# Kernel optimization log

Hardware: AMD Instinct MI355X
Metric: run time of the kernel (lower is better)

## Reference

```python
import jax, jax.numpy as jnp
import numpy as np

BN_EPS = 1e-5


def setup_inputs() -> dict:
    key = jax.random.key(0)
    ks = jax.random.split(key, 5)
    B, T, N, C, O, K, E = 2, 4, 50000, 32, 32, 3, 800000
    x = jax.random.normal(ks[0], (B, T, N, C), dtype=jnp.float32)
    edge_index = jax.random.randint(ks[1], (2, E), 0, N, dtype=jnp.int64)
    edge_weight = jax.random.uniform(ks[2], (E,), dtype=jnp.float32)
    W = jax.random.normal(ks[3], (K, C, O), dtype=jnp.float32) * 0.05
    bias = jnp.zeros((O,), dtype=jnp.float32)
    gamma = jnp.ones((O,), dtype=jnp.float32)
    beta = jnp.zeros((O,), dtype=jnp.float32)
    return {"x": x, "edge_index": edge_index, "edge_weight": edge_weight,
            "W": W, "bias": bias, "gamma": gamma, "beta": beta}


def reference(x, edge_index, edge_weight, W, bias, gamma, beta):
    # x: [B, T, N, C]; edge_index: [2, E]; W: [K, C, O]
    B, T, N, C = x.shape
    K = W.shape[0]
    src, dst = edge_index[0], edge_index[1]

    # Scaled Laplacian L_hat = 2L/lambda_max - I with sym norm, lambda_max=2
    # => L_hat = -D^{-1/2} A D^{-1/2} (zero diagonal), PyG ChebConv default.
    deg = jax.ops.segment_sum(edge_weight, src, num_segments=N)
    safe = jnp.where(deg > 0, deg, 1.0)
    dinv = jnp.where(deg > 0, 1.0 / jnp.sqrt(safe), 0.0)
    norm = -dinv[src] * edge_weight * dinv[dst]  # [E]

    # Batch all (b, t) slices together: [N, M, C] with M = B*T
    xn = jnp.transpose(x, (2, 0, 1, 3)).reshape(N, B * T, C)

    def lap(z):  # sparse SpMM applied to every (b,t) slice at once
        return jax.ops.segment_sum(norm[:, None, None] * z[src], dst,
                                   num_segments=N)

    # Chebyshev recursion: T0 = x, T1 = L_hat x, Tk = 2 L_hat T_{k-1} - T_{k-2}
    Tx_prev2 = xn
    out = jnp.einsum('nmc,co->nmo', Tx_prev2, W[0])
    if K > 1:
        Tx_prev = lap(xn)
        out = out + jnp.einsum('nmc,co->nmo', Tx_prev, W[1])
        for k in range(2, K):
            Tx_k = 2.0 * lap(Tx_prev) - Tx_prev2
            out = out + jnp.einsum('nmc,co->nmo', Tx_k, W[k])
            Tx_prev2, Tx_prev = Tx_prev, Tx_k
    out = out + bias  # [N, M, O]

    # BatchNorm1d in training mode, applied per (b,t) slice over nodes,
    # exactly as the original per-slice loop does (biased variance).
    mean = jnp.mean(out, axis=0, keepdims=True)              # [1, M, O]
    var = jnp.mean((out - mean) ** 2, axis=0, keepdims=True)  # [1, M, O]
    y = gamma * (out - mean) * jax.lax.rsqrt(var + BN_EPS) + beta
    y = jax.nn.relu(y)

    return jnp.transpose(y.reshape(N, B, T, -1), (1, 2, 0, 3))  # [B,T,N,O]
```

## Files before the change

### kernel.cpp

```cpp
#include <hip/hip_runtime.h>

#define NNODES 50000
#define NEDGES 800000
#define MB 8
#define CF 32
#define OF 32
#define FPN 256
#define TOTAL_OUT (MB * NNODES * OF)
#define NREP 8

#define BSH 9
#define BINW 512
#define NB ((NNODES + BINW - 1) / BINW)
#define BINCAP 9216
#define NBB 128
#define EPB (NEDGES / NBB)
#define CAPL 32
#define CH 16

typedef unsigned short ushort_t;
typedef unsigned int uint_t;
typedef __attribute__((ext_vector_type(8))) short bf16x8;
typedef __attribute__((ext_vector_type(4))) float f32x4;

__device__ __forceinline__ ushort_t f2bf(float f) {
    uint_t u = __float_as_uint(f);
    u += 0x7FFFu + ((u >> 16) & 1u);
    return (ushort_t)(u >> 16);
}
__device__ __forceinline__ float bflo(uint_t u) { return __uint_as_float(u << 16); }
__device__ __forceinline__ float bfhi(uint_t u) { return __uint_as_float(u & 0xFFFF0000u); }

__device__ __forceinline__ bool detect_is64(const int* ei) {
    int lane = threadIdx.x & 63;
    int v = ei[2 * lane + 1];
    return __ballot(v != 0) == 0ULL;
}

__global__ void __launch_bounds__(256) k_build(const int* __restrict__ ei,
                                               const float* __restrict__ w,
                                               const float* __restrict__ x,
                                               float* __restrict__ deg8,
                                               int* __restrict__ g_bin_cnt,
                                               int2* __restrict__ binbuf,
                                               ushort_t* __restrict__ xn) {
    int blk = blockIdx.x;
    int t = threadIdx.x;
    __shared__ int l_cnt[NB];
    __shared__ int2 l_buf[NB][CAPL];
    if (blk < NBB) {
        bool is64 = detect_is64(ei);
        for (int i = t; i < NB; i += 256) l_cnt[i] = 0;
        __syncthreads();
        int e0 = blk * EPB;
        int eend = e0 + EPB;
        for (int base = e0; base < eend; base += 256) {
            int e = base + t;
            if (e < eend) {
                int s = is64 ? ei[2 * e] : ei[e];
                int d = is64 ? ei[2 * (NEDGES + e)] : ei[NEDGES + e];
                float wt = w[e];
                atomicAdd(&deg8[s * NREP + ((e >> 8) & 7)], wt);
                int bin = d >> BSH;
                int2 entry;
                entry.x = s | ((d & (BINW - 1)) << 16);
                entry.y = __float_as_int(wt);
                int pos = atomicAdd(&l_cnt[bin], 1);
                if (pos < CAPL) {
                    l_buf[bin][pos] = entry;
                } else {
                    int gp = atomicAdd(&g_bin_cnt[bin], 1);
                    if (gp < BINCAP) binbuf[(size_t)bin * BINCAP + gp] = entry;
                }
            }
            __syncthreads();
            bool last = (base + 256 >= eend);
            if (t < NB) {
                int c = min(l_cnt[t], CAPL);
                int nflush = last ? c : (c & ~(CH - 1));
                if (nflush > 0) {
                    int gp = atomicAdd(&g_bin_cnt[t], nflush);
                    int2* dst = binbuf + (size_t)t * BINCAP;
                    for (int i = 0; i < nflush; i++) {
                        int p = gp + i;
                        if (p < BINCAP) dst[p] = l_buf[t][i];
                    }
                }
                int r = c - nflush;
                for (int i = 0; i < r; i++) l_buf[t][i] = l_buf[t][nflush + i];
                l_cnt[t] = r;
            }
            __syncthreads();
        }
    } else {
        int bb = blk - NBB;
        int lane = t & 63;
        int n = bb * 4 + (t >> 6);
        int m = lane >> 3;
        int c = (4 * lane) & 31;
        const float4 v = *(const float4*)(x + ((size_t)m * NNODES + n) * CF + c);
        uint2 d;
        d.x = (uint_t)f2bf(v.x) | ((uint_t)f2bf(v.y) << 16);
        d.y = (uint_t)f2bf(v.z) | ((uint_t)f2bf(v.w) << 16);
        *(uint2*)(xn + (size_t)n * FPN + 4 * lane) = d;
    }
}

__global__ void __launch_bounds__(256) k_csr(const int* __restrict__ g_bin_cnt,
                                             const int2* __restrict__ binbuf,
                                             int2* __restrict__ csr,
                                             int* __restrict__ csr_off) {
    __shared__ int l_ncnt[BINW];
    __shared__ int l_off[BINW];
    __shared__ int l_ws[4];
    __shared__ int l_red[4];
    int b = blockIdx.x;
    int t = threadIdx.x;
    int lane = t & 63, wv = t >> 6;

    int vb = (t < b) ? min(g_bin_cnt[t], BINCAP) : 0;
    #pragma unroll
    for (int off = 32; off >= 1; off >>= 1) vb += __shfl_down(vb, off);
    if (lane == 0) l_red[wv] = vb;
    l_ncnt[t] = 0;
    l_ncnt[t + 256] = 0;
    __syncthreads();
    int base = l_red[0] + l_red[1] + l_red[2] + l_red[3];

    int cnt = min(g_bin_cnt[b], BINCAP);
    const int2* bp = binbuf + (size_t)b * BINCAP;
    for (int i = t; i < cnt; i += 256) {
        int dl = bp[i].x >> 16;
        atomicAdd(&l_ncnt[dl], 1);
    }
    __syncthreads();

    int a0 = l_ncnt[2 * t], a1 = l_ncnt[2 * t + 1];
    int psum = a0 + a1;
    int v = psum;
    #pragma unroll
    for (int off = 1; off < 64; off <<= 1) {
        int u = __shfl_up(v, off);
        if (lane >= off) v += u;
    }
    if (lane == 63) l_ws[wv] = v;
    __syncthreads();
    int wpre = 0;
    for (int i = 0; i < wv; i++) wpre += l_ws[i];
    int excl = wpre + v - psum;
    l_off[2 * t] = excl;
    l_off[2 * t + 1] = excl + a0;
    __syncthreads();

    int n0 = b * BINW;
    for (int i = t; i < BINW; i += 256) {
        int n = n0 + i;
        if (n < NNODES) csr_off[n] = base + l_off[i];
    }
    if (b == NB - 1 && t == 0) csr_off[NNODES] = base + cnt;
    __syncthreads();

    for (int i = t; i < cnt; i += 256) {
        int2 e = bp[i];
        int dl = e.x >> 16;
        int slot = atomicAdd(&l_off[dl], 1);
        int2 o;
        o.x = e.x & 0xFFFF;
        o.y = e.y;
        csr[(size_t)base + slot] = o;
    }
}

__global__ void k_dinv(const float* __restrict__ deg8, float* __restrict__ dinv) {
    int n = blockIdx.x * blockDim.x + threadIdx.x;
    if (n >= NNODES) return;
    const float4* p = (const float4*)(deg8 + (size_t)n * NREP);
    float4 a = p[0], b = p[1];
    float s = a.x + a.y + a.z + a.w + b.x + b.y + b.z + b.w;
    dinv[n] = (s > 0.0f) ? (1.0f / sqrtf(s)) : 0.0f;
}

template <int PHASE>
__global__ void __launch_bounds__(256) k_spmm(const ushort_t* __restrict__ src,
                                              const ushort_t* __restrict__ xn0,
                                              const int* __restrict__ csr_off,
                                              const int2* __restrict__ csr,
                                              const float* __restrict__ dinv,
                                              ushort_t* __restrict__ dst) {
    int t = threadIdx.x;
    int lane = t & 63;
    int n = __builtin_amdgcn_readfirstlane(blockIdx.x * 4 + (t >> 6));
    int off = csr_off[n];
    int cnt = min(csr_off[n + 1] - off, 64);
    float dn = dinv[n];
    float a0 = 0.0f, a1 = 0.0f, a2 = 0.0f, a3 = 0.0f;
    if (cnt > 0) {
        int j = off + min(lane, cnt - 1);
        int2 ed = csr[j];
        int cv = ed.x;
        float vw = -dinv[cv] * __int_as_float(ed.y) * dn;
        uint_t vv = __float_as_uint(vw);
        for (int k = 0; k < cnt; k += 16) {
            int sc[16]; float v[16];
            #pragma unroll
            for (int i = 0; i < 16; i++) {
                sc[i] = __builtin_amdgcn_readlane(cv, k + i);
                float vr = __uint_as_float(__builtin_amdgcn_readlane((int)vv, k + i));
                v[i] = (k + i < cnt) ? vr : 0.0f;
            }
            uint2 u[16];
            #pragma unroll
            for (int i = 0; i < 16; i++)
                u[i] = *(const uint2*)(src + (size_t)sc[i] * FPN + 4 * lane);
            #pragma unroll
            for (int i = 0; i < 16; i++) {
                a0 += v[i] * bflo(u[i].x);
                a1 += v[i] * bfhi(u[i].x);
                a2 += v[i] * bflo(u[i].y);
                a3 += v[i] * bfhi(u[i].y);
            }
        }
    }
    if (PHASE == 2) {
        const uint2 xu = *(const uint2*)(xn0 + (size_t)n * FPN + 4 * lane);
        a0 = 2.0f * a0 - bflo(xu.x);
        a1 = 2.0f * a1 - bfhi(xu.x);
        a2 = 2.0f * a2 - bflo(xu.y);
        a3 = 2.0f * a3 - bfhi(xu.y);
    }
    uint2 d;
    d.x = (uint_t)f2bf(a0) | ((uint_t)f2bf(a1) << 16);
    d.y = (uint_t)f2bf(a2) | ((uint_t)f2bf(a3) << 16);
    *(uint2*)(dst + (size_t)n * FPN + 4 * lane) = d;
}

__global__ void k_wprep(const float* __restrict__ W, ushort_t* __restrict__ wbf) {
    int tid = threadIdx.x;
    for (int i = tid; i < 384; i += 256) {
        int k    = i >> 7;
        int rem  = i & 127;
        int oh   = rem >> 6;
        int lane = rem & 63;
        int quad = lane >> 4;
        int colc = lane & 15;
        ushort_t* d = wbf + (size_t)i * 8;
        for (int j = 0; j < 8; j++) {
            int c = quad * 8 + j;
            int o = oh * 16 + colc;
            d[j] = f2bf(W[k * (CF * OF) + c * OF + o]);
        }
    }
}

__global__ void __launch_bounds__(256) k_wfuse(const ushort_t* __restrict__ xn,
                                               const ushort_t* __restrict__ t1,
                                               const ushort_t* __restrict__ t2,
                                               const ushort_t* __restrict__ wbf,
                                               const float* __restrict__ bias,
                                               float* __restrict__ out) {
    int t = threadIdx.x;
    int lane = t & 63;
    int wv = blockIdx.x * 4 + (t >> 6);
    if (wv >= NNODES / 16) return;
    int n0 = wv * 16;
    int quad = lane >> 4, col = lane & 15;

    bf16x8 B[6];
    #pragma unroll
    for (int i = 0; i < 6; i++)
        B[i] = *(const bf16x8*)(wbf + (size_t)(i * 64 + lane) * 8);
    float blo = bias[col], bhi = bias[16 + col];

    size_t aoff = (size_t)(n0 + col) * FPN + quad * 8;
    #pragma unroll
    for (int m = 0; m < 8; m++) {
        bf16x8 A0 = *(const bf16x8*)(xn + aoff + m * 32);
        bf16x8 A1 = *(const bf16x8*)(t1 + aoff + m * 32);
        bf16x8 A2 = *(const bf16x8*)(t2 + aoff + m * 32);
        f32x4 lo = { blo, blo, blo, blo };
        f32x4 hi = { bhi, bhi, bhi, bhi };
        lo = __builtin_amdgcn_mfma_f32_16x16x32_bf16(A0, B[0], lo, 0, 0, 0);
        hi = __builtin_amdgcn_mfma_f32_16x16x32_bf16(A0, B[1], hi, 0, 0, 0);
        lo = __builtin_amdgcn_mfma_f32_16x16x32_bf16(A1, B[2], lo, 0, 0, 0);
        hi = __builtin_amdgcn_mfma_f32_16x16x32_bf16(A1, B[3], hi, 0, 0, 0);
        lo = __builtin_amdgcn_mfma_f32_16x16x32_bf16(A2, B[4], lo, 0, 0, 0);
        hi = __builtin_amdgcn_mfma_f32_16x16x32_bf16(A2, B[5], hi, 0, 0, 0);
        float* ob = out + ((size_t)m * NNODES + n0 + quad * 4) * OF + col;
        #pragma unroll
        for (int r = 0; r < 4; r++) {
            ob[(size_t)r * OF]      = lo[r];
            ob[(size_t)r * OF + 16] = hi[r];
        }
    }
}

__global__ void __launch_bounds__(256) k_stats(const float* __restrict__ out,
                                               float* __restrict__ stats) {
    int m = blockIdx.y;
    int t = threadIdx.x;
    int o4 = t & 7, row = t >> 3;
    int n0 = blockIdx.x * 1024;
    int nend = min(n0 + 1024, NNODES);
    float sx = 0, sy = 0, sz = 0, sw = 0;
    float qx = 0, qy = 0, qz = 0, qw = 0;
    for (int n = n0 + row; n < nend; n += 32) {
        const float4 v = *(const float4*)(out + ((size_t)m * NNODES + n) * OF + o4 * 4);
        sx += v.x; sy += v.y; sz += v.z; sw += v.w;
        qx += v.x * v.x; qy += v.y * v.y; qz += v.z * v.z; qw += v.w * v.w;
    }
    __shared__ float4 sS[256];
    __shared__ float4 sQ[256];
    sS[t] = make_float4(sx, sy, sz, sw);
    sQ[t] = make_float4(qx, qy, qz, qw);
    __syncthreads();
    for (int off = 16; off >= 1; off >>= 1) {
        if (row < off) {
            float4 a = sS[t], b = sS[t + off * 8];
            sS[t] = make_float4(a.x + b.x, a.y + b.y, a.z + b.z, a.w + b.w);
            float4 c = sQ[t], d = sQ[t + off * 8];
            sQ[t] = make_float4(c.x + d.x, c.y + d.y, c.z + d.z, c.w + d.w);
        }
        __syncthreads();
    }
    if (row == 0) {
        float4 s = sS[t], q = sQ[t];
        int base = m * 32 + o4 * 4;
        atomicAdd(&stats[base + 0], s.x);
        atomicAdd(&stats[base + 1], s.y);
        atomicAdd(&stats[base + 2], s.z);
        atomicAdd(&stats[base + 3], s.w);
        atomicAdd(&stats[256 + base + 0], q.x);
        atomicAdd(&stats[256 + base + 1], q.y);
        atomicAdd(&stats[256 + base + 2], q.z);
        atomicAdd(&stats[256 + base + 3], q.w);
    }
}

__global__ void __launch_bounds__(256) k_final(float* __restrict__ out,
                                               const float* __restrict__ stats,
                                               const float* __restrict__ gamma,
                                               const float* __restrict__ beta) {
    int idx4 = blockIdx.x * 256 + threadIdx.x;
    size_t base = (size_t)idx4 * 4;
    int o = (int)(base & 31);
    int m = (int)(base / ((size_t)NNODES * OF));
    int mo = m * 32 + o;
    const float4 sm = *(const float4*)(stats + mo);
    const float4 sq = *(const float4*)(stats + 256 + mo);
    const float4 g  = *(const float4*)(gamma + o);
    const float4 bt = *(const float4*)(beta + o);
    const float inv_n = 1.0f / (float)NNODES;
    float4 v = *(const float4*)(out + base);
    {
        float mean = sm.x * inv_n, var = sq.x * inv_n - mean * mean;
        float sc = g.x * rsqrtf(var + 1e-5f);
        v.x = fmaxf(v.x * sc + (bt.x - sc * mean), 0.0f);
    }
    {
        float mean = sm.y * inv_n, var = sq.y * inv_n - mean * mean;
        float sc = g.y * rsqrtf(var + 1e-5f);
        v.y = fmaxf(v.y * sc + (bt.y - sc * mean), 0.0f);
    }
    {
        float mean = sm.z * inv_n, var = sq.z * inv_n - mean * mean;
        float sc = g.z * rsqrtf(var + 1e-5f);
        v.z = fmaxf(v.z * sc + (bt.z - sc * mean), 0.0f);
    }
    {
        float mean = sm.w * inv_n, var = sq.w * inv_n - mean * mean;
        float sc = g.w * rsqrtf(var + 1e-5f);
        v.w = fmaxf(v.w * sc + (bt.w - sc * mean), 0.0f);
    }
    *(float4*)(out + base) = v;
}

extern "C" void kernel_launch(void* const* d_in, const int* in_sizes, int n_in,
                              void* d_out, int out_size, void* d_ws, size_t ws_size,
                              hipStream_t stream) {
    const float* x     = (const float*)d_in[0];
    const int*   ei    = (const int*)d_in[1];
    const float* w     = (const float*)d_in[2];
    const float* W     = (const float*)d_in[3];
    const float* bias  = (const float*)d_in[4];
    const float* gamma = (const float*)d_in[5];
    const float* beta  = (const float*)d_in[6];
    float* out = (float*)d_out;

    char* p = (char*)d_ws;
    auto alloc = [&](size_t bytes) {
        char* r = p;
        p += (bytes + 511) & ~(size_t)511;
        return r;
    };
    int*      g_bin_cnt = (int*)alloc((size_t)NB * 4);
    float*    deg8   = (float*)alloc((size_t)NNODES * NREP * 4);
    float*    stats  = (float*)alloc(512 * 4);
    float*    dinv   = (float*)alloc((size_t)NNODES * 4);
    int2*     binbuf = (int2*)alloc((size_t)NB * BINCAP * 8);
    int2*     csr    = (int2*)alloc((size_t)NEDGES * 8);
    int*      csr_off= (int*)alloc((size_t)(NNODES + 1) * 4);
    ushort_t* wbf    = (ushort_t*)alloc(384 * 8 * 2);
    ushort_t* xn     = (ushort_t*)alloc((size_t)NNODES * FPN * 2);
    ushort_t* t1     = (ushort_t*)alloc((size_t)NNODES * FPN * 2);
    ushort_t* t2     = (ushort_t*)alloc((size_t)NNODES * FPN * 2);

    size_t zlen = (char*)(stats + 512) - (char*)g_bin_cnt;
    hipMemsetAsync(g_bin_cnt, 0, zlen, stream);

    k_wprep<<<1, 256, 0, stream>>>(W, wbf);
    k_build<<<NBB + NNODES / 4, 256, 0, stream>>>(ei, w, x, deg8, g_bin_cnt, binbuf, xn);
    k_dinv<<<(NNODES + 255) / 256, 256, 0, stream>>>(deg8, dinv);
    k_csr<<<NB, 256, 0, stream>>>(g_bin_cnt, binbuf, csr, csr_off);

    k_spmm<1><<<NNODES / 4, 256, 0, stream>>>(xn, xn, csr_off, csr, dinv, t1);
    k_spmm<2><<<NNODES / 4, 256, 0, stream>>>(t1, xn, csr_off, csr, dinv, t2);

    int wfblocks = (NNODES / 16 + 3) / 4;
    k_wfuse<<<wfblocks, 256, 0, stream>>>(xn, t1, t2, wbf, bias, out);

    dim3 sgrid((NNODES + 1023) / 1024, MB);
    k_stats<<<sgrid, 256, 0, stream>>>(out, stats);
    k_final<<<TOTAL_OUT / 4 / 256, 256, 0, stream>>>(out, stats, gamma, beta);
}
```

Measured before the change: 392.1 us.

## Spread edge binning over more blocks and flush local bins in parallel

```diff
diff --git a/kernel.cpp b/kernel.cpp
--- a/kernel.cpp
+++ b/kernel.cpp
@@ -12,11 +12,12 @@
 #define BSH 9
 #define BINW 512
 #define NB ((NNODES + BINW - 1) / BINW)
-#define BINCAP 9216
-#define NBB 128
-#define EPB (NEDGES / NBB)
-#define CAPL 32
+#define NBA 512
+#define EPB ((NEDGES + NBA - 1) / NBA)
+#define CAPL 38
+#define LBW 48
 #define CH 16
+#define BINCAP 14336
 
 typedef unsigned short ushort_t;
 typedef unsigned int uint_t;
@@ -41,59 +42,69 @@
                                                const float* __restrict__ w,
                                                const float* __restrict__ x,
                                                float* __restrict__ deg8,
-                                               int* __restrict__ g_bin_cnt,
-                                               int2* __restrict__ binbuf,
+                                               int* __restrict__ g_cnt,
+                                               int* __restrict__ g_real,
+                                               int2* __restrict__ binD,
                                                ushort_t* __restrict__ xn) {
     int blk = blockIdx.x;
     int t = threadIdx.x;
     __shared__ int l_cnt[NB];
-    __shared__ int2 l_buf[NB][CAPL];
-    if (blk < NBB) {
+    __shared__ int l_base[NB];
+    __shared__ int l_pfx[NB + 1];
+    __shared__ int2 l_buf[NB][LBW];
+    if (blk < NBA) {
         bool is64 = detect_is64(ei);
         for (int i = t; i < NB; i += 256) l_cnt[i] = 0;
         __syncthreads();
         int e0 = blk * EPB;
-        int eend = e0 + EPB;
-        for (int base = e0; base < eend; base += 256) {
-            int e = base + t;
-            if (e < eend) {
-                int s = is64 ? ei[2 * e] : ei[e];
-                int d = is64 ? ei[2 * (NEDGES + e)] : ei[NEDGES + e];
-                float wt = w[e];
-                atomicAdd(&deg8[s * NREP + ((e >> 8) & 7)], wt);
-                int bin = d >> BSH;
-                int2 entry;
-                entry.x = s | ((d & (BINW - 1)) << 16);
-                entry.y = __float_as_int(wt);
-                int pos = atomicAdd(&l_cnt[bin], 1);
-                if (pos < CAPL) {
-                    l_buf[bin][pos] = entry;
-                } else {
-                    int gp = atomicAdd(&g_bin_cnt[bin], 1);
-                    if (gp < BINCAP) binbuf[(size_t)bin * BINCAP + gp] = entry;
-                }
+        int e1 = min(e0 + EPB, NEDGES);
+        for (int e = e0 + t; e < e1; e += 256) {
+            int s = is64 ? ei[2 * e] : ei[e];
+            int d = is64 ? ei[2 * (NEDGES + e)] : ei[NEDGES + e];
+            float wt = w[e];
+            atomicAdd(&deg8[s * NREP + ((e >> 8) & 7)], wt);
+            int bin = d >> BSH;
+            int2 entry;
+            entry.x = s | ((d & (BINW - 1)) << 16);
+            entry.y = __float_as_int(wt);
+            int pos = atomicAdd(&l_cnt[bin], 1);
+            if (pos < CAPL) {
+                l_buf[bin][pos] = entry;
+            } else {
+                int gp = atomicAdd(&g_cnt[bin], 1);
+                if (gp < BINCAP) binD[(size_t)bin * BINCAP + gp] = entry;
+                atomicAdd(&g_real[bin], 1);
             }
-            __syncthreads();
-            bool last = (base + 256 >= eend);
-            if (t < NB) {
-                int c = min(l_cnt[t], CAPL);
-                int nflush = last ? c : (c & ~(CH - 1));
-                if (nflush > 0) {
-                    int gp = atomicAdd(&g_bin_cnt[t], nflush);
-                    int2* dst = binbuf + (size_t)t * BINCAP;
-                    for (int i = 0; i < nflush; i++) {
-                        int p = gp + i;
-                        if (p < BINCAP) dst[p] = l_buf[t][i];
-                    }
-                }
-                int r = c - nflush;
-                for (int i = 0; i < r; i++) l_buf[t][i] = l_buf[t][nflush + i];
-                l_cnt[t] = r;
+        }
+        __syncthreads();
+        if (t < NB) {
+            int c = min(l_cnt[t], CAPL);
+            int p = (c + CH - 1) & ~(CH - 1);
+            for (int i = c; i < p; i++) l_buf[t][i] = make_int2(0, 0);
+            l_cnt[t] = p;
+            if (p > 0) l_base[t] = atomicAdd(&g_cnt[t], p);
+            if (c > 0) atomicAdd(&g_real[t], c);
+        }
+        __syncthreads();
+        if (t == 0) {
+            int sacc = 0;
+            for (int b2 = 0; b2 < NB; b2++) { l_pfx[b2] = sacc; sacc += l_cnt[b2]; }
+            l_pfx[NB] = sacc;
+        }
+        __syncthreads();
+        int total = l_pfx[NB];
+        for (int idx = t; idx < total; idx += 256) {
+            int lo = 0, hi = NB - 1;
+            while (lo < hi) {
+                int mid = (lo + hi + 1) >> 1;
+                if (l_pfx[mid] <= idx) lo = mid; else hi = mid - 1;
             }
-            __syncthreads();
+            int rel = idx - l_pfx[lo];
+            int gp = l_base[lo] + rel;
+            if (gp < BINCAP) binD[(size_t)lo * BINCAP + gp] = l_buf[lo][rel];
         }
     } else {
-        int bb = blk - NBB;
+        int bb = blk - NBA;
         int lane = t & 63;
         int n = bb * 4 + (t >> 6);
         int m = lane >> 3;
@@ -106,10 +117,20 @@
     }
 }
 
-__global__ void __launch_bounds__(256) k_csr(const int* __restrict__ g_bin_cnt,
-                                             const int2* __restrict__ binbuf,
-                                             int2* __restrict__ csr,
-                                             int* __restrict__ csr_off) {
+__global__ void k_dinv(const float* __restrict__ deg8, float* __restrict__ dinv) {
+    int n = blockIdx.x * blockDim.x + threadIdx.x;
+    if (n >= NNODES) return;
+    const float4* p = (const float4*)(deg8 + (size_t)n * NREP);
+    float4 a = p[0], b = p[1];
+    float s = a.x + a.y + a.z + a.w + b.x + b.y + b.z + b.w;
+    dinv[n] = (s > 0.0f) ? (1.0f / sqrtf(s)) : 0.0f;
+}
+
+__global__ void __launch_bounds__(256) k_pass2(const int* __restrict__ g_cnt,
+                                               const int* __restrict__ g_real,
+                                               const int2* __restrict__ binD,
+                                               int2* __restrict__ csr,
+                                               int* __restrict__ csr_off) {
     __shared__ int l_ncnt[BINW];
     __shared__ int l_off[BINW];
     __shared__ int l_ws[4];
@@ -118,7 +139,7 @@
     int t = threadIdx.x;
     int lane = t & 63, wv = t >> 6;
 
-    int vb = (t < b) ? min(g_bin_cnt[t], BINCAP) : 0;
+    int vb = (t < b) ? min(g_real[t], BINCAP) : 0;
     #pragma unroll
     for (int off = 32; off >= 1; off >>= 1) vb += __shfl_down(vb, off);
     if (lane == 0) l_red[wv] = vb;
@@ -127,11 +148,11 @@
     __syncthreads();
     int base = l_red[0] + l_red[1] + l_red[2] + l_red[3];
 
-    int cnt = min(g_bin_cnt[b], BINCAP);
-    const int2* bp = binbuf + (size_t)b * BINCAP;
+    int cnt = min(g_cnt[b], BINCAP);
+    const int2* bp = binD + (size_t)b * BINCAP;
     for (int i = t; i < cnt; i += 256) {
-        int dl = bp[i].x >> 16;
-        atomicAdd(&l_ncnt[dl], 1);
+        int2 e = bp[i];
+        if (e.y != 0) atomicAdd(&l_ncnt[e.x >> 16], 1);
     }
     __syncthreads();
 
@@ -157,27 +178,18 @@
         int n = n0 + i;
         if (n < NNODES) csr_off[n] = base + l_off[i];
     }
-    if (b == NB - 1 && t == 0) csr_off[NNODES] = base + cnt;
+    if (b == NB - 1 && t == 0)
+        csr_off[NNODES] = base + l_ws[0] + l_ws[1] + l_ws[2] + l_ws[3];
     __syncthreads();
 
     for (int i = t; i < cnt; i += 256) {
         int2 e = bp[i];
-        int dl = e.x >> 16;
-        int slot = atomicAdd(&l_off[dl], 1);
-        int2 o;
-        o.x = e.x & 0xFFFF;
-        o.y = e.y;
-        csr[(size_t)base + slot] = o;
-    }
-}
-
-__global__ void k_dinv(const float* __restrict__ deg8, float* __restrict__ dinv) {
-    int n = blockIdx.x * blockDim.x + threadIdx.x;
-    if (n >= NNODES) return;
-    const float4* p = (const float4*)(deg8 + (size_t)n * NREP);
-    float4 a = p[0], b = p[1];
-    float s = a.x + a.y + a.z + a.w + b.x + b.y + b.z + b.w;
-    dinv[n] = (s > 0.0f) ? (1.0f / sqrtf(s)) : 0.0f;
+        if (e.y != 0) {
+            int dl = e.x >> 16;
+            int slot = atomicAdd(&l_off[dl], 1);
+            csr[(size_t)base + slot] = make_int2(e.x & 0xFFFF, e.y);
+        }
+    }
 }
 
 template <int PHASE>
@@ -392,25 +404,27 @@
         p += (bytes + 511) & ~(size_t)511;
         return r;
     };
-    int*      g_bin_cnt = (int*)alloc((size_t)NB * 4);
-    float*    deg8   = (float*)alloc((size_t)NNODES * NREP * 4);
-    float*    stats  = (float*)alloc(512 * 4);
-    float*    dinv   = (float*)alloc((size_t)NNODES * 4);
-    int2*     binbuf = (int2*)alloc((size_t)NB * BINCAP * 8);
-    int2*     csr    = (int2*)alloc((size_t)NEDGES * 8);
-    int*      csr_off= (int*)alloc((size_t)(NNODES + 1) * 4);
-    ushort_t* wbf    = (ushort_t*)alloc(384 * 8 * 2);
-    ushort_t* xn     = (ushort_t*)alloc((size_t)NNODES * FPN * 2);
-    ushort_t* t1     = (ushort_t*)alloc((size_t)NNODES * FPN * 2);
-    ushort_t* t2     = (ushort_t*)alloc((size_t)NNODES * FPN * 2);
-
-    size_t zlen = (char*)(stats + 512) - (char*)g_bin_cnt;
-    hipMemsetAsync(g_bin_cnt, 0, zlen, stream);
+    int*      g_cnt   = (int*)alloc((size_t)NB * 4);
+    int*      g_real  = (int*)alloc((size_t)NB * 4);
+    float*    stats   = (float*)alloc(512 * 4);
+    float*    deg8    = (float*)alloc((size_t)NNODES * NREP * 4);
+    float*    dinv    = (float*)alloc((size_t)NNODES * 4);
+    int2*     binD    = (int2*)alloc((size_t)NB * BINCAP * 8);
+    int2*     csr     = (int2*)alloc((size_t)NEDGES * 8);
+    int*      csr_off = (int*)alloc((size_t)(NNODES + 1) * 4);
+    ushort_t* wbf     = (ushort_t*)alloc(384 * 8 * 2);
+    ushort_t* xn      = (ushort_t*)alloc((size_t)NNODES * FPN * 2);
+    ushort_t* t1      = (ushort_t*)alloc((size_t)NNODES * FPN * 2);
+    ushort_t* t2      = (ushort_t*)alloc((size_t)NNODES * FPN * 2);
+
+    size_t zlen = (char*)(deg8 + (size_t)NNODES * NREP) - (char*)g_cnt;
+    hipMemsetAsync(g_cnt, 0, zlen, stream);
 
     k_wprep<<<1, 256, 0, stream>>>(W, wbf);
-    k_build<<<NBB + NNODES / 4, 256, 0, stream>>>(ei, w, x, deg8, g_bin_cnt, binbuf, xn);
+    k_build<<<NBA + NNODES / 4, 256, 0, stream>>>(ei, w, x, deg8, g_cnt, g_real,
+                                                  binD, xn);
     k_dinv<<<(NNODES + 255) / 256, 256, 0, stream>>>(deg8, dinv);
-    k_csr<<<NB, 256, 0, stream>>>(g_bin_cnt, binbuf, csr, csr_off);
+    k_pass2<<<NB, 256, 0, stream>>>(g_cnt, g_real, binD, csr, csr_off);
 
     k_spmm<1><<<NNODES / 4, 256, 0, stream>>>(xn, xn, csr_off, csr, dinv, t1);
     k_spmm<2><<<NNODES / 4, 256, 0, stream>>>(t1, xn, csr_off, csr, dinv, t2);
```

Result: faster. 373.9 us (-4.6%).
